# Kernel optimization log

Hardware: AMD Instinct MI355X
Metric: run time of the kernel (lower is better)

Reference implementation:

```python
import jax, jax.numpy as jnp
import numpy as np

B, C, T = 32, 64, 1024        # batch_size, in_channels, cycle_size
H, D = 2, 64                  # GATv2 heads, per-head dim (dim_h)
DIM2 = H * D                  # dim_h * 2 = 128
K = 9                         # temporal_kernel_size
N = B * T                     # graph nodes after flatten
E = 524288                    # edges (avg degree 16)
EPS = 1e-5


def bn3d(x, gamma, beta):
    # BatchNorm1d on [B, C, T] in training mode (batch statistics)
    mu = x.mean(axis=(0, 2), keepdims=True)
    var = x.var(axis=(0, 2), keepdims=True)
    xn = (x - mu) * jax.lax.rsqrt(var + EPS)
    return xn * gamma[None, :, None] + beta[None, :, None]


def bn2d(x, gamma, beta):
    # BatchNorm1d on [N, C] in training mode
    mu = x.mean(axis=0, keepdims=True)
    var = x.var(axis=0, keepdims=True)
    return (x - mu) * jax.lax.rsqrt(var + EPS) * gamma + beta


def conv1d_same(x, w, b):
    # x: [B, Cin, T], w: [Cout, Cin, K]
    y = jax.lax.conv_general_dilated(x, w, (1,), 'SAME',
                                     dimension_numbers=('NCH', 'OIH', 'NCH'))
    return y + b[None, :, None]


def gatv2(x, edge_index, wl, wr, att, bias):
    # PyG GATv2Conv defaults: heads=H, concat=True, leaky slope 0.2, self-loops
    loops = jnp.arange(N, dtype=edge_index.dtype)
    src = jnp.concatenate([edge_index[0], loops])
    dst = jnp.concatenate([edge_index[1], loops])
    xl = (x @ wl.T).reshape(N, H, D)   # source transform
    xr = (x @ wr.T).reshape(N, H, D)   # target transform
    m = jax.nn.leaky_relu(xl[src] + xr[dst], 0.2)        # [E+N, H, D]
    logits = jnp.einsum('ehd,hd->eh', m, att)            # [E+N, H]
    lmax = jax.ops.segment_max(logits, dst, num_segments=N)
    lmax = jax.lax.stop_gradient(jnp.where(jnp.isfinite(lmax), lmax, 0.0))
    p = jnp.exp(logits - lmax[dst])
    denom = jax.ops.segment_sum(p, dst, num_segments=N)  # >0: self-loops
    alpha = p / denom[dst]                               # softmax over in-edges
    out = jax.ops.segment_sum(xl[src] * alpha[:, :, None], dst, num_segments=N)
    return out.reshape(N, DIM2) + bias


def setup_inputs() -> dict:
    key = jax.random.key(0)
    ks = jax.random.split(key, 10)
    s = lambda k, shape: jax.random.normal(k, shape, jnp.float32) * 0.05
    return {
        'x': jax.random.normal(ks[0], (B, C, T), jnp.float32),
        'edge_index': jax.random.randint(ks[1], (2, E), 0, N, jnp.int32),
        'bn0_gamma': jnp.ones((C,), jnp.float32),
        'bn0_beta': jnp.zeros((C,), jnp.float32),
        'conv_w': s(ks[2], (DIM2, C, K)),
        'conv_b': s(ks[3], (DIM2,)),
        'gat_wl': s(ks[4], (DIM2, C)),
        'gat_wr': s(ks[5], (DIM2, C)),
        'gat_att': s(ks[6], (H, D)),
        'gat_bias': s(ks[7], (DIM2,)),
        'bn1_gamma': jnp.ones((DIM2,), jnp.float32),
        'bn1_beta': jnp.zeros((DIM2,), jnp.float32),
        'cheb_w': s(ks[8], (DIM2, DIM2)),
        'cheb_b': s(ks[9], (DIM2,)),
        'train': 0,
    }


def reference(x, edge_index, bn0_gamma, bn0_beta, conv_w, conv_b,
              gat_wl, gat_wr, gat_att, gat_bias, bn1_gamma, bn1_beta,
              cheb_w, cheb_b, train):
    x = bn3d(x, bn0_gamma, bn0_beta)                       # b0 (batch_size > 1)
    residual = jax.nn.relu(conv1d_same(x, conv_w, conv_b)) # skip_connection
    h = x.reshape(T * B, C)                                # flatten to nodes
    h = gatv2(h, edge_index, gat_wl, gat_wr, gat_att, gat_bias)
    h = jax.nn.relu(bn2d(h, bn1_gamma, bn1_beta))          # b1
    h = h.reshape(B, DIM2, T)
    h = residual + h
    # chain of views: (T*B,d) -> (B,d,T) -> (B,T,-1) -> (T*B,d); pure reshapes
    h = h.reshape(T * B, DIM2)
    h = h @ cheb_w.T + cheb_b                              # ChebConv K=1 == linear
    h = jax.nn.relu(bn2d(h, bn1_gamma, bn1_beta))          # b1 again
    h = h.reshape(B, DIM2, T)
    return residual + h                                    # dropout: identity (eval)
```

## Files before the change

kernel.cpp:

```cpp
#include <hip/hip_runtime.h>

#define DEVINL __device__ __forceinline__

constexpr int Bc = 32, Cc = 64, Tc = 1024, DIM2c = 128;
constexpr int Nn = Bc * Tc;
constexpr int Ec = 524288;

typedef __bf16 bf16x8 __attribute__((ext_vector_type(8)));
typedef float  f32x4  __attribute__((ext_vector_type(4)));

constexpr long O_RES   = 0;
constexpr long O_GOUT  = 4194304;
constexpr long O_XLQ   = 10485760;
constexpr long O_XRQ   = 12582912;
constexpr long O_Z     = 16777216;
constexpr long O_WCBF  = 20971520;
constexpr long O_WLR   = 21008384;
constexpr long O_CHB   = 21016576;
constexpr long O_STAT  = 21024768;
constexpr long O_CUR   = 21025792;
constexpr long O_BUCK  = 21058560;

DEVINL float unpack_lo(unsigned v) { return __uint_as_float(v << 16); }
DEVINL float unpack_hi(unsigned v) { return __uint_as_float(v & 0xffff0000u); }
DEVINL unsigned bfb(float f) { return (__float_as_uint(f) + 0x8000u) >> 16; }
DEVINL unsigned pk2(float lo, float hi) {
    return ((__float_as_uint(hi) + 0x8000u) & 0xffff0000u) | bfb(lo);
}

__global__ __launch_bounds__(256) void setup(const float* __restrict__ x,
        const float* __restrict__ cw, const float* __restrict__ wl,
        const float* __restrict__ wr, const float* __restrict__ chw,
        const int* __restrict__ ei,
        __bf16* __restrict__ wcbf, __bf16* __restrict__ wlrbf,
        __bf16* __restrict__ chwbf,
        float* __restrict__ sum0, float* __restrict__ sq0,
        int* __restrict__ cursor, int* __restrict__ bucket) {
    int bid = blockIdx.x, tid = threadIdx.x;
    if (bid < 416) {
        int i = bid * 256 + tid;
        if (i < 73728) {
            int kk = i >> 13, co = (i >> 6) & 127, ci = i & 63;
            wcbf[i] = (__bf16)cw[co * 576 + ci * 9 + kk];
        } else if (i < 73728 + 16384) {
            int j = i - 73728;
            int r = j >> 6, c = j & 63;
            float v = (r < 128) ? wl[r * 64 + c] : wr[(r - 128) * 64 + c];
            wlrbf[j] = (__bf16)v;
        } else {
            int j = i - 73728 - 16384;
            chwbf[j] = (__bf16)chw[j];
        }
    } else if (bid < 672) {
        int pq = bid - 416;
        int c = pq & 63, q = pq >> 6;
        const float4* base = (const float4*)(x + (long)q * 8 * 65536 + (long)c * 1024);
        float s = 0.f, qq = 0.f;
        for (int i = tid; i < 2048; i += 256) {
            int b = i >> 8, t4 = i & 255;
            float4 v = base[b * 16384 + t4];
            s += v.x + v.y + v.z + v.w;
            qq = fmaf(v.x, v.x, qq); qq = fmaf(v.y, v.y, qq);
            qq = fmaf(v.z, v.z, qq); qq = fmaf(v.w, v.w, qq);
        }
        for (int off = 32; off; off >>= 1) { s += __shfl_down(s, off); qq += __shfl_down(qq, off); }
        __shared__ float ls[4], lq[4];
        int w = tid >> 6, lane = tid & 63;
        if (lane == 0) { ls[w] = s; lq[w] = qq; }
        __syncthreads();
        if (tid == 0) {
            unsafeAtomicAdd(sum0 + c, ls[0] + ls[1] + ls[2] + ls[3]);
            unsafeAtomicAdd(sq0 + c, lq[0] + lq[1] + lq[2] + lq[3]);
        }
    } else {
        int e = (bid - 672) * 256 + tid;
        int t = ei[Ec + e];
        int slot = atomicAdd(cursor + t, 1);
        bucket[t * 64 + slot] = ei[e];
    }
}

__global__ __launch_bounds__(256) void gemm1_bn0(const float* __restrict__ x,
        const float* __restrict__ sum0, const float* __restrict__ sq0,
        const float* __restrict__ g0, const float* __restrict__ b0,
        const __bf16* __restrict__ wlrbf,
        unsigned short* __restrict__ xl16, unsigned short* __restrict__ xr16) {
    __shared__ __align__(16) __bf16 as_[64 * 72];
    int tid = threadIdx.x;
    int mb = blockIdx.x;
    int b = mb >> 4, ci0 = (mb & 15) * 4;
    const float4* x4 = (const float4*)(x + (long)b * 65536 + (long)ci0 * 1024);
    #pragma unroll
    for (int it = 0; it < 4; it++) {
        int ci = ci0 + it;
        float mu = sum0[ci] * (1.f / 32768.f);
        float var = sq0[ci] * (1.f / 32768.f) - mu * mu;
        float sc = rsqrtf(var + 1e-5f) * g0[ci];
        float sh = b0[ci] - mu * sc;
        float4 v = x4[it * 256 + tid];
        int row = it * 16 + (tid >> 4);
        int col = (tid & 15) * 4;
        __bf16* p = as_ + row * 72 + col;
        p[0] = (__bf16)fmaf(v.x, sc, sh);
        p[1] = (__bf16)fmaf(v.y, sc, sh);
        p[2] = (__bf16)fmaf(v.z, sc, sh);
        p[3] = (__bf16)fmaf(v.w, sc, sh);
    }
    __syncthreads();
    int wv = tid >> 6, lane = tid & 63;
    int col = lane & 15, q = lane >> 4;
    int d0 = wv * 16;
    long mbase = (long)mb * 64;
    bf16x8 bfr[4][2];
    #pragma unroll
    for (int t = 0; t < 4; t++) {
        int j = d0 + t * 64 + col;
        #pragma unroll
        for (int ks = 0; ks < 2; ks++)
            bfr[t][ks] = *(const bf16x8*)(wlrbf + (long)j * 64 + ks * 32 + q * 8);
    }
    int d = d0 + col;
    for (int mt = 0; mt < 4; mt++) {
        const __bf16* ap = as_ + (mt * 16 + col) * 72;
        bf16x8 a0 = *(const bf16x8*)(ap + q * 8);
        bf16x8 a1 = *(const bf16x8*)(ap + 32 + q * 8);
        f32x4 acc[4];
        #pragma unroll
        for (int t = 0; t < 4; t++) { acc[t][0] = 0.f; acc[t][1] = 0.f; acc[t][2] = 0.f; acc[t][3] = 0.f; }
        #pragma unroll
        for (int t = 0; t < 4; t++) {
            acc[t] = __builtin_amdgcn_mfma_f32_16x16x32_bf16(a0, bfr[t][0], acc[t], 0, 0, 0);
            acc[t] = __builtin_amdgcn_mfma_f32_16x16x32_bf16(a1, bfr[t][1], acc[t], 0, 0, 0);
        }
        long r0 = mbase + mt * 16;
        #pragma unroll
        for (int reg = 0; reg < 4; reg++) {
            long rb = (r0 + q * 4 + reg) * 128;
            xl16[rb + d]      = (unsigned short)bfb(acc[0][reg]);
            xl16[rb + 64 + d] = (unsigned short)bfb(acc[1][reg]);
            xr16[rb + d]      = (unsigned short)bfb(acc[2][reg]);
            xr16[rb + 64 + d] = (unsigned short)bfb(acc[3][reg]);
        }
    }
}

constexpr int XS_STRIDE = 72;

DEVINL void conv_role(int cid, const float* __restrict__ x,
        const float* __restrict__ sum0, const float* __restrict__ sq0,
        const float* __restrict__ g0, const float* __restrict__ b0,
        const __bf16* __restrict__ wcbf, const float* __restrict__ cb,
        float* __restrict__ res, __bf16* xs, float* scs, float* shs) {
    int tid = threadIdx.x;
    int tbase = (cid & 7) * 128;
    int cohalf = (cid >> 3) & 1;
    int b = cid >> 4;
    if (tid < 64) {
        float mu = sum0[tid] * (1.f / 32768.f);
        float var = sq0[tid] * (1.f / 32768.f) - mu * mu;
        float sc = rsqrtf(var + 1e-5f) * g0[tid];
        scs[tid] = sc; shs[tid] = b0[tid] - mu * sc;
    }
    __syncthreads();
    int w = tid >> 6, lane = tid & 63;
    const float* xb = x + (long)b * 65536;
    for (int cc = 0; cc < 16; cc++) {
        int ci = w * 16 + cc;
        float sc = scs[ci], sh = shs[ci];
        const float* xp = xb + ci * 1024 + tbase - 4;
        #pragma unroll
        for (int rp = 0; rp < 2; rp++) {
            int rr = rp * 64 + lane;
            int t = tbase - 4 + rr;
            float v = 0.f;
            if ((unsigned)t < 1024u) v = fmaf(xp[rr], sc, sh);
            xs[rr * XS_STRIDE + ci] = (__bf16)v;
        }
        if (lane < 8) {
            int rr = 128 + lane;
            int t = tbase - 4 + rr;
            float v = 0.f;
            if ((unsigned)t < 1024u) v = fmaf(xp[rr], sc, sh);
            xs[rr * XS_STRIDE + ci] = (__bf16)v;
        }
    }
    __syncthreads();
    int col = lane & 15, q = lane >> 4;
    int co0 = cohalf * 64 + w * 16;
    bf16x8 af[18];
    #pragma unroll
    for (int kk = 0; kk < 9; kk++)
        #pragma unroll
        for (int ks = 0; ks < 2; ks++)
            af[kk * 2 + ks] = *(const bf16x8*)(wcbf +
                ((long)kk * 8192 + (long)(co0 + col) * 64 + ks * 32 + q * 8));
    float bi0 = cb[co0 + q * 4], bi1 = cb[co0 + q * 4 + 1];
    float bi2 = cb[co0 + q * 4 + 2], bi3 = cb[co0 + q * 4 + 3];
    for (int nt = 0; nt < 8; nt++) {
        int t0 = tbase + nt * 16;
        f32x4 acc; acc[0] = bi0; acc[1] = bi1; acc[2] = bi2; acc[3] = bi3;
        #pragma unroll
        for (int kk = 0; kk < 9; kk++) {
            const __bf16* rp = xs + (nt * 16 + col + kk) * XS_STRIDE + q * 8;
            #pragma unroll
            for (int ks = 0; ks < 2; ks++) {
                bf16x8 bfx = *(const bf16x8*)(rp + ks * 32);
                acc = __builtin_amdgcn_mfma_f32_16x16x32_bf16(af[kk * 2 + ks], bfx, acc, 0, 0, 0);
            }
        }
        long ob = (long)b * 131072 + (long)(co0 + q * 4) * 1024 + t0 + col;
        res[ob]        = fmaxf(acc[0], 0.f);
        res[ob + 1024] = fmaxf(acc[1], 0.f);
        res[ob + 2048] = fmaxf(acc[2], 0.f);
        res[ob + 3072] = fmaxf(acc[3], 0.f);
    }
}

DEVINL void gat_role(int wvid, const uint4* __restrict__ xlq4,
        const uint4* __restrict__ xrq4,
        const int* __restrict__ cursor, const int* __restrict__ bucket,
        const float* __restrict__ att, unsigned* __restrict__ goutb) {
    int lane = threadIdx.x & 63;
    int g = lane >> 3, j = lane & 7;
    int n = wvid * 8 + g;
    float av[16];
    #pragma unroll
    for (int k = 0; k < 16; k++) av[k] = att[16 * j + k];
    uint4 r0v = xrq4[(long)n * 16 + j * 2];
    uint4 r1v = xrq4[(long)n * 16 + j * 2 + 1];
    float xr[16];
    {
        unsigned ru[8] = {r0v.x, r0v.y, r0v.z, r0v.w, r1v.x, r1v.y, r1v.z, r1v.w};
        #pragma unroll
        for (int k = 0; k < 8; k++) { xr[2*k] = unpack_lo(ru[k]); xr[2*k+1] = unpack_hi(ru[k]); }
    }
    int cnt = cursor[n];
    const int* bk = bucket + (long)n * 64;
    int mx = cnt;
    mx = max(mx, __shfl_xor(mx, 8));
    mx = max(mx, __shfl_xor(mx, 16));
    mx = max(mx, __shfl_xor(mx, 32));
    float acc[16];
    #pragma unroll
    for (int k = 0; k < 16; k++) acc[k] = 0.f;
    float den = 0.f;
    int s0 = (0 < cnt) ? bk[0] : n;
    uint4 p0 = xlq4[(long)s0 * 16 + j * 2];
    uint4 p1 = xlq4[(long)s0 * 16 + j * 2 + 1];
    int s_next = (1 < cnt) ? bk[1] : n;
    for (int it = 0; it <= mx; it++) {
        uint4 c0 = p0, c1 = p1;
        int sn = s_next;
        int i2 = it + 2;
        s_next = (i2 < cnt) ? bk[i2] : n;
        if (it < mx) {
            p0 = xlq4[(long)sn * 16 + j * 2];
            p1 = xlq4[(long)sn * 16 + j * 2 + 1];
        }
        unsigned uu[8] = {c0.x, c0.y, c0.z, c0.w, c1.x, c1.y, c1.z, c1.w};
        float xl[16];
        float w = 0.f;
        #pragma unroll
        for (int k = 0; k < 8; k++) {
            float lo = unpack_lo(uu[k]), hi = unpack_hi(uu[k]);
            xl[2*k] = lo; xl[2*k+1] = hi;
            float s0f = lo + xr[2*k]; s0f = fmaxf(s0f, 0.2f * s0f);
            float s1f = hi + xr[2*k+1]; s1f = fmaxf(s1f, 0.2f * s1f);
            w = fmaf(s1f, av[2*k+1], fmaf(s0f, av[2*k], w));
        }
        w += __shfl_xor(w, 1); w += __shfl_xor(w, 2);
        float e2 = (it <= cnt) ? __expf(w) : 0.f;
        den += e2;
        #pragma unroll
        for (int k = 0; k < 16; k++) acc[k] = fmaf(e2, xl[k], acc[k]);
    }
    float rn = __builtin_amdgcn_rcpf(den);
    uint4 o0, o1;
    o0.x = pk2(acc[0] * rn, acc[1] * rn);
    o0.y = pk2(acc[2] * rn, acc[3] * rn);
    o0.z = pk2(acc[4] * rn, acc[5] * rn);
    o0.w = pk2(acc[6] * rn, acc[7] * rn);
    o1.x = pk2(acc[8] * rn, acc[9] * rn);
    o1.y = pk2(acc[10] * rn, acc[11] * rn);
    o1.z = pk2(acc[12] * rn, acc[13] * rn);
    o1.w = pk2(acc[14] * rn, acc[15] * rn);
    *(uint4*)(goutb + (long)n * 64 + 8 * j)     = o0;
    *(uint4*)(goutb + (long)n * 64 + 8 * j + 4) = o1;
}

__global__ __launch_bounds__(256) void conv_gat(const float* __restrict__ x,
        const float* __restrict__ sum0, const float* __restrict__ sq0,
        const float* __restrict__ g0, const float* __restrict__ b0,
        const __bf16* __restrict__ wcbf, const float* __restrict__ cb,
        float* __restrict__ res,
        const uint4* __restrict__ xlq4, const uint4* __restrict__ xrq4,
        const int* __restrict__ cursor, const int* __restrict__ bucket,
        const float* __restrict__ att, unsigned* __restrict__ goutb) {
    __shared__ __align__(16) __bf16 xs[136 * XS_STRIDE];
    __shared__ float scs[64], shs[64];
    int bid = blockIdx.x;
    if (bid < 512)
        conv_role(bid, x, sum0, sq0, g0, b0, wcbf, cb, res, xs, scs, shs);
    else
        gat_role((bid - 512) * 4 + ((int)threadIdx.x >> 6),
                 xlq4, xrq4, cursor, bucket, att, goutb);
}

__global__ __launch_bounds__(256) void bn_stats_bf(const unsigned* __restrict__ G,
        float* __restrict__ sum, float* __restrict__ sq) {
    int c = threadIdx.x & 63, sub = threadIdx.x >> 6;
    int r0 = blockIdx.x * 128;
    float sl = 0.f, sh = 0.f, ql = 0.f, qh = 0.f;
    for (int r = r0 + sub; r < r0 + 128; r += 4) {
        unsigned v = G[(long)r * 64 + c];
        float lo = unpack_lo(v), hi = unpack_hi(v);
        sl += lo; ql = fmaf(lo, lo, ql);
        sh += hi; qh = fmaf(hi, hi, qh);
    }
    __shared__ float A[256], B[256], C[256], D[256];
    A[threadIdx.x] = sl; B[threadIdx.x] = sh;
    C[threadIdx.x] = ql; D[threadIdx.x] = qh;
    __syncthreads();
    if (threadIdx.x < 64) {
        int t = threadIdx.x;
        float s_lo = A[t] + A[t + 64] + A[t + 128] + A[t + 192];
        float s_hi = B[t] + B[t + 64] + B[t + 128] + B[t + 192];
        float q_lo = C[t] + C[t + 64] + C[t + 128] + C[t + 192];
        float q_hi = D[t] + D[t + 64] + D[t + 128] + D[t + 192];
        unsafeAtomicAdd(sum + 2 * t,     s_lo);
        unsafeAtomicAdd(sum + 2 * t + 1, s_hi);
        unsafeAtomicAdd(sq  + 2 * t,     q_lo);
        unsafeAtomicAdd(sq  + 2 * t + 1, q_hi);
    }
}

__global__ __launch_bounds__(256) void cheb_fused(const unsigned* __restrict__ goutb,
        const float* __restrict__ res, const float* __restrict__ sum1,
        const float* __restrict__ sq1, const float* __restrict__ g1,
        const float* __restrict__ b1, const __bf16* __restrict__ chwbf,
        unsigned* __restrict__ zb, float* __restrict__ sum2, float* __restrict__ sq2) {
    __shared__ unsigned xsu[64 * 68];
    __shared__ float scs[128], shs[128], cs[128], cq[128];
    int tid = threadIdx.x;
    if (tid < 128) {
        float mu = sum1[tid] * (1.f / 32768.f);
        float var = sq1[tid] * (1.f / 32768.f) - mu * mu;
        float rs = rsqrtf(var + 1e-5f);
        float sc = rs * g1[tid];
        scs[tid] = sc; shs[tid] = b1[tid] - mu * sc;
        cs[tid] = 0.f;
    } else cq[tid - 128] = 0.f;
    __syncthreads();
    long r0 = (long)blockIdx.x * 64;
    for (int i = tid; i < 2048; i += 256) {
        int row = i >> 5, c4 = i & 31;
        long gidx = (r0 + row) * 32 + c4;
        uint2 gv = ((const uint2*)goutb)[gidx];
        float4 r = ((const float4*)res)[gidx];
        int f0 = c4 * 4;
        float v0 = unpack_lo(gv.x), v1 = unpack_hi(gv.x);
        float v2 = unpack_lo(gv.y), v3 = unpack_hi(gv.y);
        float o0 = r.x + fmaxf(fmaf(v0, scs[f0],     shs[f0]),     0.f);
        float o1 = r.y + fmaxf(fmaf(v1, scs[f0 + 1], shs[f0 + 1]), 0.f);
        float o2 = r.z + fmaxf(fmaf(v2, scs[f0 + 2], shs[f0 + 2]), 0.f);
        float o3 = r.w + fmaxf(fmaf(v3, scs[f0 + 3], shs[f0 + 3]), 0.f);
        xsu[row * 68 + c4 * 2]     = pk2(o0, o1);
        xsu[row * 68 + c4 * 2 + 1] = pk2(o2, o3);
    }
    __syncthreads();
    int wv = tid >> 6, lane = tid & 63;
    int col = lane & 15, q = lane >> 4;
    bf16x8 bfr[2][4];
    #pragma unroll
    for (int t = 0; t < 2; t++) {
        int jj = wv * 16 + t * 64 + col;
        #pragma unroll
        for (int ks = 0; ks < 4; ks++)
            bfr[t][ks] = *(const bf16x8*)(chwbf + (long)jj * 128 + ks * 32 + q * 8);
    }
    float ls0 = 0.f, ls1 = 0.f, lq0 = 0.f, lq1 = 0.f;
    bool evenc = (col & 1) == 0;
    int fpair0 = (wv * 16 + col) >> 1;
    for (int mt = 0; mt < 4; mt++) {
        const __bf16* ap = (const __bf16*)xsu + (mt * 16 + col) * 136;
        bf16x8 a[4];
        #pragma unroll
        for (int ks = 0; ks < 4; ks++)
            a[ks] = *(const bf16x8*)(ap + ks * 32 + q * 8);
        f32x4 acc[2];
        #pragma unroll
        for (int t = 0; t < 2; t++) { acc[t][0] = 0.f; acc[t][1] = 0.f; acc[t][2] = 0.f; acc[t][3] = 0.f; }
        #pragma unroll
        for (int t = 0; t < 2; t++)
            #pragma unroll
            for (int ks = 0; ks < 4; ks++)
                acc[t] = __builtin_amdgcn_mfma_f32_16x16x32_bf16(a[ks], bfr[t][ks], acc[t], 0, 0, 0);
        #pragma unroll
        for (int reg = 0; reg < 4; reg++) {
            float v0 = acc[0][reg], v1 = acc[1][reg];
            ls0 += v0; lq0 = fmaf(v0, v0, lq0);
            ls1 += v1; lq1 = fmaf(v1, v1, lq1);
            float n0 = __shfl_xor(v0, 1);
            float n1 = __shfl_xor(v1, 1);
            if (evenc) {
                long zrow = (r0 + mt * 16 + q * 4 + reg) * 64;
                zb[zrow + fpair0]      = pk2(v0, n0);
                zb[zrow + 32 + fpair0] = pk2(v1, n1);
            }
        }
    }
    int j0 = wv * 16 + col;
    atomicAdd(&cs[j0], ls0);      atomicAdd(&cs[j0 + 64], ls1);
    atomicAdd(&cq[j0], lq0);      atomicAdd(&cq[j0 + 64], lq1);
    __syncthreads();
    if (tid < 128) unsafeAtomicAdd(sum2 + tid, cs[tid]);
    else unsafeAtomicAdd(sq2 + tid - 128, cq[tid - 128]);
}

__global__ __launch_bounds__(256) void bn_res(const unsigned* __restrict__ zb,
        const float* __restrict__ res, const float* __restrict__ sum,
        const float* __restrict__ sq, const float* __restrict__ g,
        const float* __restrict__ bta, float* __restrict__ out) {
    __shared__ float scs[128], shs[128];
    int tid = threadIdx.x;
    if (tid < 128) {
        float mu = sum[tid] * (1.f / 32768.f);
        float var = sq[tid] * (1.f / 32768.f) - mu * mu;
        float rs = rsqrtf(var + 1e-5f);
        float sc = rs * g[tid];
        scs[tid] = sc; shs[tid] = bta[tid] - mu * sc;
    }
    __syncthreads();
    int idx = blockIdx.x * 256 + tid;
    int f0 = (idx & 31) * 4;
    uint2 zv = ((const uint2*)zb)[idx];
    float4 r = ((const float4*)res)[idx];
    float v0 = unpack_lo(zv.x), v1 = unpack_hi(zv.x);
    float v2 = unpack_lo(zv.y), v3 = unpack_hi(zv.y);
    float4 o;
    o.x = r.x + fmaxf(fmaf(v0, scs[f0],     shs[f0]),     0.f);
    o.y = r.y + fmaxf(fmaf(v1, scs[f0 + 1], shs[f0 + 1]), 0.f);
    o.z = r.z + fmaxf(fmaf(v2, scs[f0 + 2], shs[f0 + 2]), 0.f);
    o.w = r.w + fmaxf(fmaf(v3, scs[f0 + 3], shs[f0 + 3]), 0.f);
    ((float4*)out)[idx] = o;
}

extern "C" void kernel_launch(void* const* d_in, const int* in_sizes, int n_in,
                              void* d_out, int out_size, void* d_ws, size_t ws_size,
                              hipStream_t stream) {
    const float* x   = (const float*)d_in[0];
    const int*   ei  = (const int*)d_in[1];
    const float* g0  = (const float*)d_in[2];
    const float* b0  = (const float*)d_in[3];
    const float* cw  = (const float*)d_in[4];
    const float* cb  = (const float*)d_in[5];
    const float* wl  = (const float*)d_in[6];
    const float* wr  = (const float*)d_in[7];
    const float* att = (const float*)d_in[8];
    const float* g1  = (const float*)d_in[10];
    const float* b1  = (const float*)d_in[11];
    const float* chw = (const float*)d_in[12];
    float* out = (float*)d_out;

    float* ws = (float*)d_ws;
    float*    res   = ws + O_RES;
    unsigned* goutb = (unsigned*)(ws + O_GOUT);
    unsigned* xlq   = (unsigned*)(ws + O_XLQ);
    unsigned* xrq   = (unsigned*)(ws + O_XRQ);
    unsigned* zb    = (unsigned*)(ws + O_Z);
    __bf16*   wcbf  = (__bf16*)(ws + O_WCBF);
    __bf16*   wlrbf = (__bf16*)(ws + O_WLR);
    __bf16*   chwbf = (__bf16*)(ws + O_CHB);
    float*    st    = ws + O_STAT;
    int*      cursor = (int*)(ws + O_CUR);
    int*      bucket = (int*)(ws + O_BUCK);
    float *sum0 = st,       *sq0 = st + 64;
    float *sum1 = st + 128, *sq1 = st + 256;
    float *sum2 = st + 384, *sq2 = st + 512;

    hipMemsetAsync(st, 0, (size_t)(1024 + 32768) * 4, stream);

    setup<<<2720, 256, 0, stream>>>(x, cw, wl, wr, chw, ei,
                                    wcbf, wlrbf, chwbf, sum0, sq0, cursor, bucket);
    gemm1_bn0<<<512, 256, 0, stream>>>(x, sum0, sq0, g0, b0, wlrbf,
                                       (unsigned short*)xlq, (unsigned short*)xrq);
    conv_gat<<<1536, 256, 0, stream>>>(x, sum0, sq0, g0, b0, wcbf, cb, res,
                                       (const uint4*)xlq, (const uint4*)xrq,
                                       cursor, bucket, att, goutb);
    bn_stats_bf<<<256, 256, 0, stream>>>(goutb, sum1, sq1);
    cheb_fused<<<512, 256, 0, stream>>>(goutb, res, sum1, sq1, g1, b1, chwbf,
                                        zb, sum2, sq2);
    bn_res<<<4096, 256, 0, stream>>>(zb, res, sum2, sq2, g1, b1, out);
}
```

Measured before the change: 221.1 us.

## Fuse BN stats, Cheb GEMM and final BN-residual into one cooperative kernel

```diff
diff --git a/kernel.cpp b/kernel.cpp
--- a/kernel.cpp
+++ b/kernel.cpp
@@ -1,4 +1,5 @@
 #include <hip/hip_runtime.h>
+#include <hip/hip_cooperative_groups.h>
 
 #define DEVINL __device__ __forceinline__
 
@@ -306,60 +307,64 @@
                  xlq4, xrq4, cursor, bucket, att, goutb);
 }
 
-__global__ __launch_bounds__(256) void bn_stats_bf(const unsigned* __restrict__ G,
-        float* __restrict__ sum, float* __restrict__ sq) {
-    int c = threadIdx.x & 63, sub = threadIdx.x >> 6;
-    int r0 = blockIdx.x * 128;
-    float sl = 0.f, sh = 0.f, ql = 0.f, qh = 0.f;
-    for (int r = r0 + sub; r < r0 + 128; r += 4) {
-        unsigned v = G[(long)r * 64 + c];
-        float lo = unpack_lo(v), hi = unpack_hi(v);
-        sl += lo; ql = fmaf(lo, lo, ql);
-        sh += hi; qh = fmaf(hi, hi, qh);
-    }
-    __shared__ float A[256], B[256], C[256], D[256];
-    A[threadIdx.x] = sl; B[threadIdx.x] = sh;
-    C[threadIdx.x] = ql; D[threadIdx.x] = qh;
-    __syncthreads();
-    if (threadIdx.x < 64) {
-        int t = threadIdx.x;
-        float s_lo = A[t] + A[t + 64] + A[t + 128] + A[t + 192];
-        float s_hi = B[t] + B[t + 64] + B[t + 128] + B[t + 192];
-        float q_lo = C[t] + C[t + 64] + C[t + 128] + C[t + 192];
-        float q_hi = D[t] + D[t + 64] + D[t + 128] + D[t + 192];
-        unsafeAtomicAdd(sum + 2 * t,     s_lo);
-        unsafeAtomicAdd(sum + 2 * t + 1, s_hi);
-        unsafeAtomicAdd(sq  + 2 * t,     q_lo);
-        unsafeAtomicAdd(sq  + 2 * t + 1, q_hi);
-    }
-}
-
-__global__ __launch_bounds__(256) void cheb_fused(const unsigned* __restrict__ goutb,
-        const float* __restrict__ res, const float* __restrict__ sum1,
-        const float* __restrict__ sq1, const float* __restrict__ g1,
+__global__ __launch_bounds__(256) void tail_fused(const unsigned* __restrict__ goutb,
+        const float* __restrict__ res, float* __restrict__ sum1,
+        float* __restrict__ sq1, const float* __restrict__ g1,
         const float* __restrict__ b1, const __bf16* __restrict__ chwbf,
-        unsigned* __restrict__ zb, float* __restrict__ sum2, float* __restrict__ sq2) {
+        unsigned* __restrict__ zb, float* __restrict__ sum2,
+        float* __restrict__ sq2, float* __restrict__ out) {
     __shared__ unsigned xsu[64 * 68];
     __shared__ float scs[128], shs[128], cs[128], cq[128];
     int tid = threadIdx.x;
+    long r0 = (long)blockIdx.x * 64;
+
+    if (tid < 128) cs[tid] = 0.f; else cq[tid - 128] = 0.f;
+    __syncthreads();
+    {
+        int c4 = tid & 31, f0 = c4 * 4;
+        float s0 = 0.f, s1 = 0.f, s2 = 0.f, s3 = 0.f;
+        float q0 = 0.f, q1 = 0.f, q2 = 0.f, q3 = 0.f;
+        #pragma unroll
+        for (int k = 0; k < 8; k++) {
+            int i = tid + k * 256;
+            int row = i >> 5;
+            uint2 gv = ((const uint2*)goutb)[(r0 + row) * 32 + c4];
+            xsu[row * 68 + c4 * 2]     = gv.x;
+            xsu[row * 68 + c4 * 2 + 1] = gv.y;
+            float v0 = unpack_lo(gv.x), v1 = unpack_hi(gv.x);
+            float v2 = unpack_lo(gv.y), v3 = unpack_hi(gv.y);
+            s0 += v0; q0 = fmaf(v0, v0, q0);
+            s1 += v1; q1 = fmaf(v1, v1, q1);
+            s2 += v2; q2 = fmaf(v2, v2, q2);
+            s3 += v3; q3 = fmaf(v3, v3, q3);
+        }
+        atomicAdd(&cs[f0], s0);     atomicAdd(&cs[f0 + 1], s1);
+        atomicAdd(&cs[f0 + 2], s2); atomicAdd(&cs[f0 + 3], s3);
+        atomicAdd(&cq[f0], q0);     atomicAdd(&cq[f0 + 1], q1);
+        atomicAdd(&cq[f0 + 2], q2); atomicAdd(&cq[f0 + 3], q3);
+    }
+    __syncthreads();
+    if (tid < 128) unsafeAtomicAdd(sum1 + tid, cs[tid]);
+    else unsafeAtomicAdd(sq1 + tid - 128, cq[tid - 128]);
+    __threadfence();
+    cooperative_groups::this_grid().sync();
+
     if (tid < 128) {
         float mu = sum1[tid] * (1.f / 32768.f);
         float var = sq1[tid] * (1.f / 32768.f) - mu * mu;
-        float rs = rsqrtf(var + 1e-5f);
-        float sc = rs * g1[tid];
+        float sc = rsqrtf(var + 1e-5f) * g1[tid];
         scs[tid] = sc; shs[tid] = b1[tid] - mu * sc;
         cs[tid] = 0.f;
     } else cq[tid - 128] = 0.f;
     __syncthreads();
-    long r0 = (long)blockIdx.x * 64;
     for (int i = tid; i < 2048; i += 256) {
         int row = i >> 5, c4 = i & 31;
-        long gidx = (r0 + row) * 32 + c4;
-        uint2 gv = ((const uint2*)goutb)[gidx];
-        float4 r = ((const float4*)res)[gidx];
+        unsigned gx = xsu[row * 68 + c4 * 2];
+        unsigned gy = xsu[row * 68 + c4 * 2 + 1];
+        float4 r = ((const float4*)res)[(r0 + row) * 32 + c4];
         int f0 = c4 * 4;
-        float v0 = unpack_lo(gv.x), v1 = unpack_hi(gv.x);
-        float v2 = unpack_lo(gv.y), v3 = unpack_hi(gv.y);
+        float v0 = unpack_lo(gx), v1 = unpack_hi(gx);
+        float v2 = unpack_lo(gy), v3 = unpack_hi(gy);
         float o0 = r.x + fmaxf(fmaf(v0, scs[f0],     shs[f0]),     0.f);
         float o1 = r.y + fmaxf(fmaf(v1, scs[f0 + 1], shs[f0 + 1]), 0.f);
         float o2 = r.z + fmaxf(fmaf(v2, scs[f0 + 2], shs[f0 + 2]), 0.f);
@@ -368,81 +373,80 @@
         xsu[row * 68 + c4 * 2 + 1] = pk2(o2, o3);
     }
     __syncthreads();
-    int wv = tid >> 6, lane = tid & 63;
-    int col = lane & 15, q = lane >> 4;
-    bf16x8 bfr[2][4];
-    #pragma unroll
-    for (int t = 0; t < 2; t++) {
-        int jj = wv * 16 + t * 64 + col;
-        #pragma unroll
-        for (int ks = 0; ks < 4; ks++)
-            bfr[t][ks] = *(const bf16x8*)(chwbf + (long)jj * 128 + ks * 32 + q * 8);
-    }
-    float ls0 = 0.f, ls1 = 0.f, lq0 = 0.f, lq1 = 0.f;
-    bool evenc = (col & 1) == 0;
-    int fpair0 = (wv * 16 + col) >> 1;
-    for (int mt = 0; mt < 4; mt++) {
-        const __bf16* ap = (const __bf16*)xsu + (mt * 16 + col) * 136;
-        bf16x8 a[4];
-        #pragma unroll
-        for (int ks = 0; ks < 4; ks++)
-            a[ks] = *(const bf16x8*)(ap + ks * 32 + q * 8);
-        f32x4 acc[2];
-        #pragma unroll
-        for (int t = 0; t < 2; t++) { acc[t][0] = 0.f; acc[t][1] = 0.f; acc[t][2] = 0.f; acc[t][3] = 0.f; }
-        #pragma unroll
-        for (int t = 0; t < 2; t++)
+    {
+        int wv = tid >> 6, lane = tid & 63;
+        int col = lane & 15, q = lane >> 4;
+        bf16x8 bfr[2][4];
+        #pragma unroll
+        for (int t = 0; t < 2; t++) {
+            int jj = wv * 16 + t * 64 + col;
             #pragma unroll
             for (int ks = 0; ks < 4; ks++)
-                acc[t] = __builtin_amdgcn_mfma_f32_16x16x32_bf16(a[ks], bfr[t][ks], acc[t], 0, 0, 0);
-        #pragma unroll
-        for (int reg = 0; reg < 4; reg++) {
-            float v0 = acc[0][reg], v1 = acc[1][reg];
-            ls0 += v0; lq0 = fmaf(v0, v0, lq0);
-            ls1 += v1; lq1 = fmaf(v1, v1, lq1);
-            float n0 = __shfl_xor(v0, 1);
-            float n1 = __shfl_xor(v1, 1);
-            if (evenc) {
-                long zrow = (r0 + mt * 16 + q * 4 + reg) * 64;
-                zb[zrow + fpair0]      = pk2(v0, n0);
-                zb[zrow + 32 + fpair0] = pk2(v1, n1);
+                bfr[t][ks] = *(const bf16x8*)(chwbf + (long)jj * 128 + ks * 32 + q * 8);
+        }
+        float ls0 = 0.f, ls1 = 0.f, lq0 = 0.f, lq1 = 0.f;
+        bool evenc = (col & 1) == 0;
+        int fpair0 = (wv * 16 + col) >> 1;
+        for (int mt = 0; mt < 4; mt++) {
+            const __bf16* ap = (const __bf16*)xsu + (mt * 16 + col) * 136;
+            bf16x8 a[4];
+            #pragma unroll
+            for (int ks = 0; ks < 4; ks++)
+                a[ks] = *(const bf16x8*)(ap + ks * 32 + q * 8);
+            f32x4 acc[2];
+            #pragma unroll
+            for (int t = 0; t < 2; t++) { acc[t][0] = 0.f; acc[t][1] = 0.f; acc[t][2] = 0.f; acc[t][3] = 0.f; }
+            #pragma unroll
+            for (int t = 0; t < 2; t++)
+                #pragma unroll
+                for (int ks = 0; ks < 4; ks++)
+                    acc[t] = __builtin_amdgcn_mfma_f32_16x16x32_bf16(a[ks], bfr[t][ks], acc[t], 0, 0, 0);
+            #pragma unroll
+            for (int reg = 0; reg < 4; reg++) {
+                float v0 = acc[0][reg], v1 = acc[1][reg];
+                ls0 += v0; lq0 = fmaf(v0, v0, lq0);
+                ls1 += v1; lq1 = fmaf(v1, v1, lq1);
+                float n0 = __shfl_xor(v0, 1);
+                float n1 = __shfl_xor(v1, 1);
+                if (evenc) {
+                    long zrow = (r0 + mt * 16 + q * 4 + reg) * 64;
+                    zb[zrow + fpair0]      = pk2(v0, n0);
+                    zb[zrow + 32 + fpair0] = pk2(v1, n1);
+                }
             }
         }
-    }
-    int j0 = wv * 16 + col;
-    atomicAdd(&cs[j0], ls0);      atomicAdd(&cs[j0 + 64], ls1);
-    atomicAdd(&cq[j0], lq0);      atomicAdd(&cq[j0 + 64], lq1);
+        int j0 = wv * 16 + col;
+        atomicAdd(&cs[j0], ls0);      atomicAdd(&cs[j0 + 64], ls1);
+        atomicAdd(&cq[j0], lq0);      atomicAdd(&cq[j0 + 64], lq1);
+    }
     __syncthreads();
     if (tid < 128) unsafeAtomicAdd(sum2 + tid, cs[tid]);
     else unsafeAtomicAdd(sq2 + tid - 128, cq[tid - 128]);
-}
-
-__global__ __launch_bounds__(256) void bn_res(const unsigned* __restrict__ zb,
-        const float* __restrict__ res, const float* __restrict__ sum,
-        const float* __restrict__ sq, const float* __restrict__ g,
-        const float* __restrict__ bta, float* __restrict__ out) {
-    __shared__ float scs[128], shs[128];
-    int tid = threadIdx.x;
+    __threadfence();
+    cooperative_groups::this_grid().sync();
+
     if (tid < 128) {
-        float mu = sum[tid] * (1.f / 32768.f);
-        float var = sq[tid] * (1.f / 32768.f) - mu * mu;
-        float rs = rsqrtf(var + 1e-5f);
-        float sc = rs * g[tid];
-        scs[tid] = sc; shs[tid] = bta[tid] - mu * sc;
-    }
-    __syncthreads();
-    int idx = blockIdx.x * 256 + tid;
-    int f0 = (idx & 31) * 4;
-    uint2 zv = ((const uint2*)zb)[idx];
-    float4 r = ((const float4*)res)[idx];
-    float v0 = unpack_lo(zv.x), v1 = unpack_hi(zv.x);
-    float v2 = unpack_lo(zv.y), v3 = unpack_hi(zv.y);
-    float4 o;
-    o.x = r.x + fmaxf(fmaf(v0, scs[f0],     shs[f0]),     0.f);
-    o.y = r.y + fmaxf(fmaf(v1, scs[f0 + 1], shs[f0 + 1]), 0.f);
-    o.z = r.z + fmaxf(fmaf(v2, scs[f0 + 2], shs[f0 + 2]), 0.f);
-    o.w = r.w + fmaxf(fmaf(v3, scs[f0 + 3], shs[f0 + 3]), 0.f);
-    ((float4*)out)[idx] = o;
+        float mu = sum2[tid] * (1.f / 32768.f);
+        float var = sq2[tid] * (1.f / 32768.f) - mu * mu;
+        float sc = rsqrtf(var + 1e-5f) * g1[tid];
+        scs[tid] = sc; shs[tid] = b1[tid] - mu * sc;
+    }
+    __syncthreads();
+    #pragma unroll
+    for (int k = 0; k < 8; k++) {
+        int idx = (blockIdx.x + k * 512) * 256 + tid;
+        int f0 = (idx & 31) * 4;
+        uint2 zv = ((const uint2*)zb)[idx];
+        float4 r = ((const float4*)res)[idx];
+        float v0 = unpack_lo(zv.x), v1 = unpack_hi(zv.x);
+        float v2 = unpack_lo(zv.y), v3 = unpack_hi(zv.y);
+        float4 o;
+        o.x = r.x + fmaxf(fmaf(v0, scs[f0],     shs[f0]),     0.f);
+        o.y = r.y + fmaxf(fmaf(v1, scs[f0 + 1], shs[f0 + 1]), 0.f);
+        o.z = r.z + fmaxf(fmaf(v2, scs[f0 + 2], shs[f0 + 2]), 0.f);
+        o.w = r.w + fmaxf(fmaf(v3, scs[f0 + 3], shs[f0 + 3]), 0.f);
+        ((float4*)out)[idx] = o;
+    }
 }
 
 extern "C" void kernel_launch(void* const* d_in, const int* in_sizes, int n_in,
@@ -487,8 +491,11 @@
     conv_gat<<<1536, 256, 0, stream>>>(x, sum0, sq0, g0, b0, wcbf, cb, res,
                                        (const uint4*)xlq, (const uint4*)xrq,
                                        cursor, bucket, att, goutb);
-    bn_stats_bf<<<256, 256, 0, stream>>>(goutb, sum1, sq1);
-    cheb_fused<<<512, 256, 0, stream>>>(goutb, res, sum1, sq1, g1, b1, chwbf,
-                                        zb, sum2, sq2);
-    bn_res<<<4096, 256, 0, stream>>>(zb, res, sum2, sq2, g1, b1, out);
-}
+    const uint4* xlq4c = (const uint4*)xlq;
+    (void)xlq4c;
+    void* targs[] = {(void*)&goutb, (void*)&res, (void*)&sum1, (void*)&sq1,
+                     (void*)&g1, (void*)&b1, (void*)&chwbf, (void*)&zb,
+                     (void*)&sum2, (void*)&sq2, (void*)&out};
+    hipLaunchCooperativeKernel((void*)tail_fused, dim3(512), dim3(256),
+                               targs, 0, stream);
+}
```

Measured after the change: 383.9 us. 1.74x slower.
